# Optimization experiments

Hardware: AMD Instinct MI355X
Metric: run time of the kernel (lower is better)

Reference implementation:

```python
import jax, jax.numpy as jnp
import numpy as np

SHAPE = (128, 128, 128)  # (D, H, W), batch_size = 1
N = 100000               # number of active voxels
CONV_CH = [(3, 64), (64, 64), (64, 96), (96, 96), (96, 128), (128, 128),
           (128, 160), (160, 160), (160, 192), (192, 192), (192, 224),
           (224, 224), (224, 256), (256, 256)]


def _lin(c, shape):
    Sz, Sy, Sx = shape
    return ((c[:, 0] * Sz + c[:, 1]) * Sy + c[:, 2]) * Sx + c[:, 3]


def _subm_pairs(coords, shape):
    # Submanifold conv indice pairs: for each active voxel and each of the
    # 27 kernel offsets, the row index of the active neighbor, or -1.
    Sz, Sy, Sx = shape
    n = coords.shape[0]
    grid = np.full(Sz * Sy * Sx, -1, np.int64)  # batch size 1 dense lookup (like self.grid)
    grid[_lin(coords, shape)] = np.arange(n)
    pairs = []
    for dz in (-1, 0, 1):
        for dy in (-1, 0, 1):
            for dx in (-1, 0, 1):
                z = coords[:, 1] + dz
                y = coords[:, 2] + dy
                x = coords[:, 3] + dx
                ok = (z >= 0) & (z < Sz) & (y >= 0) & (y < Sy) & (x >= 0) & (x < Sx)
                nl = ((coords[:, 0] * Sz + z) * Sy + y) * Sx + x
                pairs.append(np.where(ok, grid[np.clip(nl, 0, grid.size - 1)], -1))
    return np.stack(pairs)  # [27, n]


def _pool_structure(coords, shape):
    # SparseMaxPool3d(2,2): output sites = unique coords//2; inv maps each
    # input voxel to its output window.
    ns = tuple(s // 2 for s in shape)
    c2 = coords.copy()
    c2[:, 1:] = c2[:, 1:] // 2
    key = _lin(c2, ns)
    uniq, inv = np.unique(key, return_inverse=True)
    Sz, Sy, Sx = ns
    b = uniq // (Sz * Sy * Sx)
    r = uniq % (Sz * Sy * Sx)
    z = r // (Sy * Sx)
    r = r % (Sy * Sx)
    nc = np.stack([b, z, r // Sx, r % Sx], 1).astype(np.int64)
    return nc, inv, uniq.shape[0], ns


def _build_plan(coors_np):
    # Paired SubMConv3d layers share an indice_key -> same pairs per level.
    coords = coors_np.astype(np.int64)
    shape = SHAPE
    plan = []
    for lvl in range(7):
        p = jnp.asarray(_subm_pairs(coords, shape))
        plan.append(('conv', p))
        plan.append(('conv', p))
        if lvl < 6:
            coords, inv, m, shape = _pool_structure(coords, shape)
            plan.append(('pool', jnp.asarray(inv), m))
    return plan


def _subm_conv(feats, pairs, W):
    # gather -> GEMM -> accumulate, per kernel offset (W: [27, Cin, Cout])
    out = jnp.zeros((feats.shape[0], W.shape[2]), feats.dtype)
    for k in range(27):
        idx = pairs[k]
        g = jnp.where((idx >= 0)[:, None], feats[jnp.clip(idx, 0)], 0.0)
        out = out + g @ W[k]
    return out


def _forward(feats, weights, plan):
    wi = 0
    for step in plan:
        if step[0] == 'conv':
            feats = _subm_conv(feats, step[1], weights[wi])
            wi += 1
        else:
            feats = jax.ops.segment_max(feats, step[1], num_segments=step[2])
    return feats


def setup_inputs() -> dict:
    rng = np.random.default_rng(0)
    lin = rng.choice(SHAPE[0] * SHAPE[1] * SHAPE[2], size=N, replace=False)
    z = lin // (SHAPE[1] * SHAPE[2])
    r = lin % (SHAPE[1] * SHAPE[2])
    coors = np.stack([np.zeros(N, np.int32), z.astype(np.int32),
                      (r // SHAPE[2]).astype(np.int32), (r % SHAPE[2]).astype(np.int32)], 1)
    key = jax.random.key(0)
    keys = jax.random.split(key, len(CONV_CH) + 1)
    inp = {
        'features': jax.random.normal(keys[0], (N, 3), jnp.float32),
        'coors': jnp.asarray(coors),
        'batch_size': 1,
    }
    for i, (ci, co) in enumerate(CONV_CH):
        inp[f'w{i}'] = jax.random.normal(keys[i + 1], (27, ci, co), jnp.float32) * (1.0 / np.sqrt(27.0 * ci))
    return inp


def reference(features, coors, batch_size, w0, w1, w2, w3, w4, w5, w6, w7, w8, w9, w10, w11, w12, w13):
    plan = _build_plan(np.asarray(coors))
    ws = [w0, w1, w2, w3, w4, w5, w6, w7, w8, w9, w10, w11, w12, w13]
    return _forward(features, ws, plan)
```

## Files before the change

kernel.cpp:

```cpp
#include <hip/hip_runtime.h>
#include <cstdint>
#include <cstddef>


typedef __attribute__((ext_vector_type(8))) short short8v;
typedef __attribute__((ext_vector_type(4))) float f32x4;

static inline int cdiv_h(int a, int b) { return (a + b - 1) / b; }

__device__ inline unsigned short f2bf(float f) {
    unsigned int u = __builtin_bit_cast(unsigned int, f);
    u += 0x7FFFu + ((u >> 16) & 1u);
    return (unsigned short)(u >> 16);
}
__device__ inline float bf2f(unsigned short h) {
    unsigned int u = ((unsigned int)h) << 16;
    return __builtin_bit_cast(float, u);
}

__device__ inline void gload_lds16(const void* g, void* l) {
    auto gp = (const __attribute__((address_space(1))) unsigned int*)(uintptr_t)g;
    auto lp = (__attribute__((address_space(3))) unsigned int*)(uintptr_t)l;
    __builtin_amdgcn_global_load_lds(gp, lp, 16, 0, 0);
}

__device__ inline int xcd_swz(int bid, int nwg) {
    int q = nwg >> 3, r = nwg & 7;
    int x = bid & 7, idx = bid >> 3;
    return (x < r ? x * (q + 1) : r * (q + 1) + (x - r) * q) + idx;
}

__global__ void set_count_k(int* counts, int n) { counts[0] = n; }

__global__ void scatter_grid_k(const int* __restrict__ coords, const int* __restrict__ cnt,
                               int* __restrict__ grid, int S)
{
    int i = blockIdx.x * blockDim.x + threadIdx.x;
    if (i >= cnt[0]) return;
    int z = coords[i * 4 + 1], y = coords[i * 4 + 2], x = coords[i * 4 + 3];
    grid[(z * S + y) * S + x] = i;
}

__global__ void build_pairs_k(const int* __restrict__ coords, const int* __restrict__ cnt,
                              const int* __restrict__ grid, int* __restrict__ pairs_t, int S)
{
    int i = blockIdx.x * blockDim.x + threadIdx.x;
    if (i >= cnt[0]) return;
    int z = coords[i * 4 + 1], y = coords[i * 4 + 2], x = coords[i * 4 + 3];
    int4* dst = reinterpret_cast<int4*>(pairs_t + (size_t)i * 32);
#pragma unroll
    for (int g = 0; g < 7; ++g) {
        int4 q;
#pragma unroll
        for (int j = 0; j < 4; ++j) {
            int k = g * 4 + j;
            int v = -1;
            if (k < 27) {
                int nz = z + k / 9 - 1;
                int ny = y + (k / 3) % 3 - 1;
                int nx = x + k % 3 - 1;
                if (nz >= 0 && nz < S && ny >= 0 && ny < S && nx >= 0 && nx < S)
                    v = grid[(nz * S + ny) * S + nx];
            }
            ((int*)&q)[j] = v;
        }
        dst[g] = q;
    }
}

struct PackArgs {
    const float* src[13];
    unsigned short* dst[13];
    int cin[13];
    int cout[13];
    int tileStart[14];
};

__global__ __launch_bounds__(256) void pack_all_k(PackArgs pa)
{
    int g = blockIdx.x * 4 + ((int)threadIdx.x >> 6);
    int lane = (int)threadIdx.x & 63;
    if (g >= pa.tileStart[13]) return;
    int li = 0;
    while (li < 12 && g >= pa.tileStart[li + 1]) ++li;
    int tile = g - pa.tileStart[li];
    int CIN = pa.cin[li], COUT = pa.cout[li];
    int NS = CIN >> 5, NT = COUT >> 4;
    int t = tile % NT;
    int s = (tile / NT) % NS;
    int k = tile / (NT * NS);
    int kabs = s * 32 + (lane >> 4) * 8;
    int c = t * 16 + (lane & 15);
    const float* src = pa.src[li] + ((size_t)(k * CIN + kabs)) * COUT + c;
    unsigned short* dst = pa.dst[li] + (size_t)tile * 512 + lane * 8;
#pragma unroll
    for (int j = 0; j < 8; ++j) dst[j] = f2bf(src[(size_t)j * COUT]);
}

__global__ __launch_bounds__(256) void conv0_k(
    const float* __restrict__ fin, const float* __restrict__ W,
    const int* __restrict__ pairs_t, const int* __restrict__ cnt,
    unsigned short* __restrict__ fout)
{
    const int row = blockIdx.x * 16 + ((int)threadIdx.x >> 4);
    const int cg = ((int)threadIdx.x & 15) * 4;
    if (row >= cnt[0]) return;
    float a0 = 0, a1 = 0, a2 = 0, a3 = 0;
    for (int k = 0; k < 27; ++k) {
        int nb = pairs_t[(size_t)row * 32 + k];
        if (nb < 0) continue;
        const float* fr = fin + (size_t)nb * 3;
        const float* wk = W + (size_t)k * 3 * 64 + cg;
#pragma unroll
        for (int ci = 0; ci < 3; ++ci) {
            float f = fr[ci];
            float4 w = *reinterpret_cast<const float4*>(wk + ci * 64);
            a0 += f * w.x; a1 += f * w.y; a2 += f * w.z; a3 += f * w.w;
        }
    }
    size_t o = (size_t)row * 64 + cg;
    fout[o] = f2bf(a0); fout[o + 1] = f2bf(a1);
    fout[o + 2] = f2bf(a2); fout[o + 3] = f2bf(a3);
}

template <int CIN, int COUT, int RT, int CT, int GY, bool OUTF32>
__global__ __launch_bounds__(256) void conv_lds_k(
    const unsigned short* __restrict__ fin, const unsigned short* __restrict__ Wp,
    const int* __restrict__ pairs_t, const int* __restrict__ cnt,
    void* __restrict__ fout)
{
    constexpr int NS = CIN / 32, NT = COUT / 16;
    constexpr int NCH = NS * CT;
    __shared__ unsigned short sB[2][NCH * 512];

    const int lane = (int)threadIdx.x & 63;
    const int wave = (int)threadIdx.x >> 6;
    const int l15 = lane & 15, lhi = lane >> 4;
    const int M = cnt[0];

    const int lid = xcd_swz((int)blockIdx.x, (int)gridDim.x);
    const int rowBlock = lid / GY;
    const int ct0 = (lid % GY) * CT;
    const int rowBase = (rowBlock * 4 + wave) * (RT * 16);

    const unsigned short* __restrict__ finL = fin + (size_t)lhi * 8;

    f32x4 acc[RT][CT];
#pragma unroll
    for (int a = 0; a < RT; ++a)
#pragma unroll
        for (int b = 0; b < CT; ++b) acc[a][b] = (f32x4){0.f, 0.f, 0.f, 0.f};

    int  rowC[RT];
    bool rOK[RT];
#pragma unroll
    for (int rt = 0; rt < RT; ++rt) {
        int r = rowBase + rt * 16 + l15;
        rOK[rt]  = r < M;
        rowC[rt] = rOK[rt] ? r : 0;
    }

#define STAGE(K, BUF)                                                              \
    {                                                                              \
        const unsigned short* srcB = Wp + (size_t)(K) * (NS * NT * 512)            \
                                     + (size_t)lane * 8;                           \
        _Pragma("unroll") for (int ii = 0; ii < (NCH + 3) / 4; ++ii) {             \
            int idx = wave + ii * 4;                                               \
            if (idx < NCH) {                                                       \
                int s = idx / CT, tt = idx % CT;                                   \
                gload_lds16(srcB + ((size_t)s * NT + ct0 + tt) * 512,              \
                            &sB[BUF][idx * 512]);                                  \
            }                                                                      \
        }                                                                          \
    }

#define GATHER(AARR, NBARR, KT)                                                    \
    {                                                                              \
        _Pragma("unroll") for (int rt = 0; rt < RT; ++rt)                          \
            NBARR[rt] = rOK[rt] ? pairs_t[(size_t)rowC[rt] * 32 + (KT)] : -1;      \
        _Pragma("unroll") for (int s = 0; s < NS; ++s)                             \
        _Pragma("unroll") for (int rt = 0; rt < RT; ++rt) {                        \
            AARR[s][rt] = (short8v){};                                             \
            if (NBARR[rt] >= 0)                                                    \
                AARR[s][rt] = *reinterpret_cast<const short8v*>(                   \
                    finL + (size_t)NBARR[rt] * CIN + s * 32);                      \
        }                                                                          \
    }

#define COMPUTE(AARR, NBARR, BUF)                                                  \
    {                                                                              \
        int act[RT]; bool anyAct = false;                                          \
        _Pragma("unroll") for (int rt = 0; rt < RT; ++rt) {                        \
            act[rt] = __any(NBARR[rt] >= 0);                                       \
            anyAct = anyAct || (act[rt] != 0);                                     \
        }                                                                          \
        if (anyAct) {                                                              \
            const unsigned short* __restrict__ buf = sB[BUF];                      \
            _Pragma("unroll") for (int s = 0; s < NS; ++s) {                       \
                short8v bb[CT];                                                    \
                _Pragma("unroll") for (int t = 0; t < CT; ++t)                     \
                    bb[t] = *reinterpret_cast<const short8v*>(                     \
                        &buf[(s * CT + t) * 512 + lane * 8]);                      \
                _Pragma("unroll") for (int rt = 0; rt < RT; ++rt) {                \
                    if (!act[rt]) continue;                                        \
                    _Pragma("unroll") for (int t = 0; t < CT; ++t)                 \
                        acc[rt][t] = __builtin_amdgcn_mfma_f32_16x16x32_bf16(      \
                            AARR[s][rt], bb[t], acc[rt][t], 0, 0, 0);              \
                }                                                                  \
            }                                                                      \
        }                                                                          \
    }

    int nbP[RT], nbQ[RT];
    short8v aP[NS][RT], aQ[NS][RT];

    GATHER(aP, nbP, 0);
    STAGE(0, 0);

    for (int kk = 0; kk < 13; ++kk) {
        const int k1 = 2 * kk + 1;
        __syncthreads();
        STAGE(k1, 1);
        GATHER(aQ, nbQ, k1);
        COMPUTE(aP, nbP, 0);
        __syncthreads();
        STAGE(k1 + 1, 0);
        GATHER(aP, nbP, k1 + 1);
        COMPUTE(aQ, nbQ, 1);
    }
    __syncthreads();
    COMPUTE(aP, nbP, 0);

#undef STAGE
#undef GATHER
#undef COMPUTE

#pragma unroll
    for (int rt = 0; rt < RT; ++rt) {
#pragma unroll
        for (int j = 0; j < 4; ++j) {
            int r = rowBase + rt * 16 + lhi * 4 + j;
            if (r >= M) continue;
#pragma unroll
            for (int t = 0; t < CT; ++t) {
                int c = (ct0 + t) * 16 + l15;
                if constexpr (OUTF32)
                    ((float*)fout)[(size_t)r * COUT + c] = acc[rt][t][j];
                else
                    ((unsigned short*)fout)[(size_t)r * COUT + c] = f2bf(acc[rt][t][j]);
            }
        }
    }
}

template <int CIN, int COUT, int CTD, int TG>
__global__ __launch_bounds__(64) void conv_deep_k(
    const unsigned short* __restrict__ fin, const unsigned short* __restrict__ Wp,
    const int* __restrict__ pairs_t, const int* __restrict__ cnt,
    float* __restrict__ fout)
{
    constexpr int NS = CIN / 32, NT = COUT / 16;
    const int lane = (int)threadIdx.x;
    const int l15 = lane & 15, lhi = lane >> 4;
    const int M = cnt[0];
    if ((int)blockIdx.x * 16 >= M) return;
    const int row = blockIdx.x * 16 + l15;
    const int ct0 = blockIdx.y * CTD;
    const int k0 = blockIdx.z * TG;

    f32x4 acc[CTD];
#pragma unroll
    for (int t = 0; t < CTD; ++t) acc[t] = (f32x4){0.f, 0.f, 0.f, 0.f};

    bool anyTap = false;
#pragma unroll
    for (int kk = 0; kk < TG; ++kk) {
        const int k = k0 + kk;
        int nb = (row < M) ? pairs_t[(size_t)row * 32 + k] : -1;
        if (!__any(nb >= 0)) continue;
        anyTap = true;
        const unsigned short* wk = Wp + (size_t)k * NS * NT * 512 + (size_t)lane * 8;

        short8v a[NS];
#pragma unroll
        for (int s = 0; s < NS; ++s) {
            a[s] = (short8v){};
            if (nb >= 0)
                a[s] = *reinterpret_cast<const short8v*>(
                    fin + (size_t)nb * CIN + s * 32 + lhi * 8);
        }
#pragma unroll
        for (int s = 0; s < NS; ++s)
#pragma unroll
            for (int t = 0; t < CTD; ++t) {
                short8v b = *reinterpret_cast<const short8v*>(
                    wk + ((size_t)s * NT + ct0 + t) * 512);
                acc[t] = __builtin_amdgcn_mfma_f32_16x16x32_bf16(a[s], b, acc[t], 0, 0, 0);
            }
    }
    if (!anyTap) return;

#pragma unroll
    for (int t = 0; t < CTD; ++t)
#pragma unroll
        for (int j = 0; j < 4; ++j) {
            int r = blockIdx.x * 16 + lhi * 4 + j;
            if (r < M)
                atomicAdd(&fout[(size_t)r * COUT + (ct0 + t) * 16 + l15], acc[t][j]);
        }
}

__global__ __launch_bounds__(256) void f32_to_bf16_k(
    const float* __restrict__ src, const int* __restrict__ cnt,
    unsigned short* __restrict__ dst, int C)
{
    int idx = blockIdx.x * 256 + (int)threadIdx.x;
    if (idx / C >= cnt[0]) return;
    dst[idx] = f2bf(src[idx]);
}

__global__ void mark_occ_k(const int* __restrict__ coords, const int* __restrict__ cnt,
                           int* __restrict__ occ, int Sh)
{
    int i = blockIdx.x * blockDim.x + threadIdx.x;
    if (i >= cnt[0]) return;
    int z = coords[i * 4 + 1] >> 1, y = coords[i * 4 + 2] >> 1, x = coords[i * 4 + 3] >> 1;
    occ[(z * Sh + y) * Sh + x] = 1;
}

__global__ __launch_bounds__(256) void scan_sum_k(const int* __restrict__ occ, int P,
                                                  int* __restrict__ bsum)
{
    int base = blockIdx.x * 4096 + (int)threadIdx.x * 16;
    int s = 0;
#pragma unroll
    for (int j = 0; j < 16; ++j) { int i = base + j; s += (i < P) ? occ[i] : 0; }
    for (int off = 1; off < 64; off <<= 1) s += __shfl_xor(s, off);
    __shared__ int ws[4];
    if ((threadIdx.x & 63) == 0) ws[threadIdx.x >> 6] = s;
    __syncthreads();
    if (threadIdx.x == 0) bsum[blockIdx.x] = ws[0] + ws[1] + ws[2] + ws[3];
}

__global__ void scan_offsets_k(const int* __restrict__ bsum, int nb,
                               int* __restrict__ boff, int* __restrict__ cntOut)
{
    int lane = threadIdx.x;
    int v = (lane < nb) ? bsum[lane] : 0;
    int incl = v;
    for (int off = 1; off < 64; off <<= 1) {
        int t = __shfl_up(incl, off);
        if (lane >= off) incl += t;
    }
    if (lane < nb) boff[lane] = incl - v;
    if (lane == 63) cntOut[0] = incl;
}

__global__ __launch_bounds__(256) void scan_emit_k(const int* __restrict__ occ, int P,
                                                   const int* __restrict__ boff,
                                                   int* __restrict__ newcoords, int Sh)
{
    __shared__ int ws[4];
    int tid = threadIdx.x;
    int base = blockIdx.x * 4096 + tid * 16;
    int v[16];
    int s = 0;
#pragma unroll
    for (int j = 0; j < 16; ++j) { int i = base + j; v[j] = (i < P) ? occ[i] : 0; s += v[j]; }
    int mysum = s;
    int incl = s;
    for (int off = 1; off < 64; off <<= 1) {
        int t = __shfl_up(incl, off);
        if ((tid & 63) >= off) incl += t;
    }
    if ((tid & 63) == 63) ws[tid >> 6] = incl;
    __syncthreads();
    int waveOff = 0;
    for (int w = 0; w < (tid >> 6); ++w) waveOff += ws[w];
    int r = boff[blockIdx.x] + waveOff + incl - mysum;
    const int SS = Sh * Sh;
#pragma unroll
    for (int j = 0; j < 16; ++j) {
        if (v[j]) {
            int c = base + j;
            newcoords[r * 4 + 0] = 0;
            newcoords[r * 4 + 1] = c / SS;
            newcoords[r * 4 + 2] = (c % SS) / Sh;
            newcoords[r * 4 + 3] = c % Sh;
            ++r;
        }
    }
}

__global__ void pool_max_k(const unsigned short* __restrict__ fin, const int* __restrict__ gridPrev,
                           const int* __restrict__ newcoords, const int* __restrict__ cnt,
                           unsigned short* __restrict__ fout, int C, int Sprev)
{
    int idx = blockIdx.x * blockDim.x + threadIdx.x;
    int r = idx / C, c = idx % C;
    if (r >= cnt[0]) return;
    int z2 = newcoords[r * 4 + 1] * 2;
    int y2 = newcoords[r * 4 + 2] * 2;
    int x2 = newcoords[r * 4 + 3] * 2;
    float best = -3.4e38f;
    unsigned short bb = 0;
#pragma unroll
    for (int d = 0; d < 8; ++d) {
        int z = z2 + (d >> 2), y = y2 + ((d >> 1) & 1), x = x2 + (d & 1);
        int j = gridPrev[(z * Sprev + y) * Sprev + x];
        if (j >= 0) {
            unsigned short u = fin[(size_t)j * C + c];
            float f = bf2f(u);
            if (f > best) { best = f; bb = u; }
        }
    }
    fout[(size_t)r * C + c] = bb;
}


template <int CIN, int COUT, int RT, int CT, int GY, bool OUTF32>
static void launch_cl(const unsigned short* fin, const unsigned short* Wp,
                      const int* pairs_t, const int* cnt, void* fout,
                      int bound, hipStream_t stream)
{
    constexpr int NT = COUT / 16;
    static_assert(CIN % 32 == 0 && COUT % 16 == 0 && CT * GY == NT, "shape");
    dim3 g(cdiv_h(bound, RT * 64) * GY);
    conv_lds_k<CIN, COUT, RT, CT, GY, OUTF32><<<g, 256, 0, stream>>>(fin, Wp, pairs_t,
                                                                     cnt, fout);
}

template <int CIN, int COUT, int CTD, int TG>
static void launch_deep(const unsigned short* fin, const unsigned short* Wp,
                        const int* pairs_t, const int* cnt, float* acc,
                        int bound, hipStream_t stream)
{
    constexpr int NT = COUT / 16;
    static_assert(NT % CTD == 0 && 27 % TG == 0, "shape");
    dim3 g(cdiv_h(bound, 16), NT / CTD, 27 / TG);
    conv_deep_k<CIN, COUT, CTD, TG><<<g, 64, 0, stream>>>(fin, Wp, pairs_t, cnt, acc);
}

extern "C" void kernel_launch(void* const* d_in, const int* in_sizes, int n_in,
                              void* d_out, int out_size, void* d_ws, size_t ws_size,
                              hipStream_t stream)
{
    const float* feats0 = (const float*)d_in[0];
    const int*   coors  = (const int*)d_in[1];
    const float* w[14];
    for (int i = 0; i < 14; ++i) w[i] = (const float*)d_in[3 + i];
    float* out = (float*)d_out;
    const int N = in_sizes[0] / 3;

    char* p = (char*)d_ws;
    int* grid   = (int*)p; p += (size_t)128 * 128 * 128 * 4;
    int* occ    = (int*)p; p += (size_t)64 * 64 * 64 * 4;
    int* counts = (int*)p; p += 256;
    int* bsum   = (int*)p; p += 256;
    int* boff   = (int*)p; p += 256;
    int* pairs_t = (int*)p; p += (size_t)N * 32 * 4;
    int* coordsA = (int*)p; p += (size_t)N * 16;
    int* coordsB = (int*)p; p += (size_t)N * 16;
    unsigned short* featA = (unsigned short*)p; p += (size_t)N * 96 * 2;
    unsigned short* featB = (unsigned short*)p; p += (size_t)N * 96 * 2;
    float* scratch = (float*)p; p += (size_t)4096 * 192 * 4;
    unsigned short* wpBase = (unsigned short*)p;

    static const int CH[14][2] = {{3,64},{64,64},{64,96},{96,96},{96,128},{128,128},
                                  {128,160},{160,160},{160,192},{192,192},{192,224},
                                  {224,224},{224,256},{256,256}};
    unsigned short* wp[14];
    PackArgs pa;
    {
        size_t off = 0;
        int ts = 0;
        for (int i = 1; i < 14; ++i) {
            wp[i] = wpBase + off;
            off += (size_t)27 * CH[i][0] * CH[i][1];
            pa.src[i - 1] = w[i];
            pa.dst[i - 1] = wp[i];
            pa.cin[i - 1] = CH[i][0];
            pa.cout[i - 1] = CH[i][1];
            pa.tileStart[i - 1] = ts;
            ts += 27 * (CH[i][0] / 32) * (CH[i][1] / 16);
        }
        pa.tileStart[13] = ts;
    }

    int bounds[7];
    for (int l = 0; l < 7; ++l) {
        int S = 128 >> l, c = S * S * S;
        bounds[l] = N < c ? N : c;
    }

    set_count_k<<<1, 1, 0, stream>>>(counts, N);
    hipMemsetAsync(d_out, 0, (size_t)out_size * 4, stream);
    pack_all_k<<<cdiv_h(pa.tileStart[13], 4), 256, 0, stream>>>(pa);

    auto build_level = [&](const int* coordsL, int lvl) {
        int S = 128 >> lvl;
        hipMemsetAsync(grid, 0xFF, (size_t)S * S * S * 4, stream);
        int blocks = cdiv_h(bounds[lvl], 256);
        scatter_grid_k<<<blocks, 256, 0, stream>>>(coordsL, counts + lvl, grid, S);
        build_pairs_k<<<blocks, 256, 0, stream>>>(coordsL, counts + lvl, grid, pairs_t, S);
    };

    auto do_pool = [&](const int* coordsL, int lvl, const unsigned short* fin,
                       unsigned short* fout, int C, int* coordsOut) {
        int S = 128 >> lvl, Sh = S / 2, P = Sh * Sh * Sh;
        hipMemsetAsync(occ, 0, (size_t)P * 4, stream);
        mark_occ_k<<<cdiv_h(bounds[lvl], 256), 256, 0, stream>>>(coordsL, counts + lvl, occ, Sh);
        int nb = cdiv_h(P, 4096);
        scan_sum_k<<<nb, 256, 0, stream>>>(occ, P, bsum);
        scan_offsets_k<<<1, 64, 0, stream>>>(bsum, nb, boff, counts + lvl + 1);
        scan_emit_k<<<nb, 256, 0, stream>>>(occ, P, boff, coordsOut, Sh);
        int total = bounds[lvl + 1] * C;
        pool_max_k<<<cdiv_h(total, 256), 256, 0, stream>>>(fin, grid, coordsOut,
                                                           counts + lvl + 1, fout, C, S);
    };

    auto deep_conv = [&](auto launcher, const unsigned short* fin, int wi, int lvl,
                         unsigned short* dst, int COUT) {
        hipMemsetAsync(scratch, 0, (size_t)bounds[lvl] * COUT * 4, stream);
        launcher(fin, wp[wi], pairs_t, counts + lvl, scratch, bounds[lvl], stream);
        f32_to_bf16_k<<<cdiv_h(bounds[lvl] * COUT, 256), 256, 0, stream>>>(
            scratch, counts + lvl, dst, COUT);
    };

    build_level(coors, 0);
    conv0_k<<<cdiv_h(bounds[0], 16), 256, 0, stream>>>(feats0, w[0], pairs_t, counts + 0, featA);
    launch_cl<64, 64, 2, 4, 1, false>(featA, wp[1], pairs_t, counts + 0, featB, bounds[0], stream);
    do_pool(coors, 0, featB, featA, 64, coordsA);
    build_level(coordsA, 1);
    launch_cl<64, 96, 2, 6, 1, false>(featA, wp[2], pairs_t, counts + 1, featB, bounds[1], stream);
    launch_cl<96, 96, 2, 6, 1, false>(featB, wp[3], pairs_t, counts + 1, featA, bounds[1], stream);
    do_pool(coordsA, 1, featA, featB, 96, coordsB);
    build_level(coordsB, 2);
    launch_cl<96, 128, 2, 4, 2, false>(featB, wp[4], pairs_t, counts + 2, featA, bounds[2], stream);
    launch_cl<128, 128, 2, 4, 2, false>(featA, wp[5], pairs_t, counts + 2, featB, bounds[2], stream);
    do_pool(coordsB, 2, featB, featA, 128, coordsA);
    build_level(coordsA, 3);
    deep_conv(launch_deep<128, 160, 2, 3>, featA, 6, 3, featB, 160);
    deep_conv(launch_deep<160, 160, 2, 3>, featB, 7, 3, featA, 160);
    do_pool(coordsA, 3, featA, featB, 160, coordsB);
    build_level(coordsB, 4);
    deep_conv(launch_deep<160, 192, 2, 3>, featB, 8, 4, featA, 192);
    deep_conv(launch_deep<192, 192, 2, 3>, featA, 9, 4, featB, 192);
    do_pool(coordsB, 4, featB, featA, 192, coordsA);
    build_level(coordsA, 5);
    deep_conv(launch_deep<192, 224, 1, 1>, featA, 10, 5, featB, 224);
    deep_conv(launch_deep<224, 224, 1, 1>, featB, 11, 5, featA, 224);
    do_pool(coordsA, 5, featA, featB, 224, coordsB);
    build_level(coordsB, 6);
    deep_conv(launch_deep<224, 256, 1, 1>, featB, 12, 6, featA, 256);
    launch_deep<256, 256, 1, 1>(featA, wp[13], pairs_t, counts + 6, out, bounds[6], stream);
}
```

Before: 774.7 us.

## Triple-buffer weight LDS staging with counted vmcnt waits and unconditional gathers

Moves the sparse conv kernel from a double-buffered, __syncthreads-separated loop to a three-slot LDS ring for weight tiles. Weight loads and neighbour gathers for the next offset stay in flight across the barrier, using an explicit s_waitcnt vmcnt with a fixed outstanding count. Every stage and gather now issues a uniform number of loads: invalid neighbours read row 0 and are masked, and out-of-range stages write to a dummy LDS buffer, so the count holds. Blocks whose rows are all past M now exit early. In exchange the kernel uses more LDS and registers, which may lower occupancy, and it does extra wasted loads.

```diff
diff --git a/kernel.cpp b/kernel.cpp
--- a/kernel.cpp
+++ b/kernel.cpp
@@ -131,7 +131,12 @@
 {
     constexpr int NS = CIN / 32, NT = COUT / 16;
     constexpr int NCH = NS * CT;
-    __shared__ unsigned short sB[2][NCH * 512];
+    constexpr int SPW = (NCH + 3) / 4;
+    constexpr int G   = NS * RT;
+    constexpr int XW  = SPW + 2 * G + 2 * RT;
+    static_assert(XW <= 63, "vmcnt range");
+    __shared__ unsigned short sB[3][NCH * 512];
+    __shared__ unsigned short sDummy[512];
 
     const int lane = (int)threadIdx.x & 63;
     const int wave = (int)threadIdx.x >> 6;
@@ -141,6 +146,7 @@
     const int lid = xcd_swz((int)blockIdx.x, (int)gridDim.x);
     const int rowBlock = lid / GY;
     const int ct0 = (lid % GY) * CT;
+    if (rowBlock * (RT * 64) >= M) return;
     const int rowBase = (rowBlock * 4 + wave) * (RT * 16);
 
     const unsigned short* __restrict__ finL = fin + (size_t)lhi * 8;
@@ -160,79 +166,114 @@
         rowC[rt] = rOK[rt] ? r : 0;
     }
 
-#define STAGE(K, BUF)                                                              \
+#define STAGE(K, BUFP)                                                             \
     {                                                                              \
-        const unsigned short* srcB = Wp + (size_t)(K) * (NS * NT * 512)            \
+        const int kc_ = (K) > 26 ? 26 : (K);                                       \
+        const bool real_ = (K) <= 26;                                              \
+        const unsigned short* srcB = Wp + (size_t)kc_ * (NS * NT * 512)            \
                                      + (size_t)lane * 8;                           \
-        _Pragma("unroll") for (int ii = 0; ii < (NCH + 3) / 4; ++ii) {             \
+        _Pragma("unroll") for (int ii = 0; ii < SPW; ++ii) {                       \
             int idx = wave + ii * 4;                                               \
-            if (idx < NCH) {                                                       \
-                int s = idx / CT, tt = idx % CT;                                   \
-                gload_lds16(srcB + ((size_t)s * NT + ct0 + tt) * 512,              \
-                            &sB[BUF][idx * 512]);                                  \
-            }                                                                      \
+            int cidx = idx < NCH ? idx : 0;                                        \
+            int s_ = cidx / CT, tt_ = cidx % CT;                                   \
+            unsigned short* dst = (real_ && idx < NCH)                             \
+                                      ? ((BUFP) + idx * 512) : sDummy;             \
+            gload_lds16(srcB + ((size_t)s_ * NT + ct0 + tt_) * 512, dst);          \
         }                                                                          \
     }
 
-#define GATHER(AARR, NBARR, KT)                                                    \
+#define NBLOAD(NB, K)                                                              \
     {                                                                              \
+        _Pragma("unroll") for (int rt = 0; rt < RT; ++rt) {                        \
+            int t_ = pairs_t[(size_t)rowC[rt] * 32 + (K)];                         \
+            NB[rt] = rOK[rt] ? t_ : -1;                                            \
+        }                                                                          \
+    }
+
+#define GATHER(AARR, NB)                                                           \
+    {                                                                              \
+        _Pragma("unroll") for (int s_ = 0; s_ < NS; ++s_)                          \
+        _Pragma("unroll") for (int rt = 0; rt < RT; ++rt) {                        \
+            int n_ = NB[rt] < 0 ? 0 : NB[rt];                                      \
+            short8v v_ = *reinterpret_cast<const short8v*>(                        \
+                finL + (size_t)n_ * CIN + s_ * 32);                                \
+            AARR[s_][rt] = NB[rt] < 0 ? (short8v){} : v_;                          \
+        }                                                                          \
+    }
+
+#define WAITBAR                                                                    \
+    asm volatile("s_waitcnt vmcnt(%0)" :: "n"(XW) : "memory");                     \
+    __builtin_amdgcn_s_barrier();                                                  \
+    asm volatile("" ::: "memory");
+
+#define COMPUTE(AARR, ACT, BUFP)                                                   \
+    {                                                                              \
+        bool anyAct = false;                                                       \
         _Pragma("unroll") for (int rt = 0; rt < RT; ++rt)                          \
-            NBARR[rt] = rOK[rt] ? pairs_t[(size_t)rowC[rt] * 32 + (KT)] : -1;      \
-        _Pragma("unroll") for (int s = 0; s < NS; ++s)                             \
-        _Pragma("unroll") for (int rt = 0; rt < RT; ++rt) {                        \
-            AARR[s][rt] = (short8v){};                                             \
-            if (NBARR[rt] >= 0)                                                    \
-                AARR[s][rt] = *reinterpret_cast<const short8v*>(                   \
-                    finL + (size_t)NBARR[rt] * CIN + s * 32);                      \
-        }                                                                          \
-    }
-
-#define COMPUTE(AARR, NBARR, BUF)                                                  \
-    {                                                                              \
-        int act[RT]; bool anyAct = false;                                          \
-        _Pragma("unroll") for (int rt = 0; rt < RT; ++rt) {                        \
-            act[rt] = __any(NBARR[rt] >= 0);                                       \
-            anyAct = anyAct || (act[rt] != 0);                                     \
-        }                                                                          \
+            anyAct = anyAct || (ACT[rt] != 0);                                     \
         if (anyAct) {                                                              \
-            const unsigned short* __restrict__ buf = sB[BUF];                      \
-            _Pragma("unroll") for (int s = 0; s < NS; ++s) {                       \
+            const unsigned short* __restrict__ buf = (BUFP);                       \
+            _Pragma("unroll") for (int s_ = 0; s_ < NS; ++s_) {                    \
                 short8v bb[CT];                                                    \
-                _Pragma("unroll") for (int t = 0; t < CT; ++t)                     \
-                    bb[t] = *reinterpret_cast<const short8v*>(                     \
-                        &buf[(s * CT + t) * 512 + lane * 8]);                      \
+                _Pragma("unroll") for (int t_ = 0; t_ < CT; ++t_)                  \
+                    bb[t_] = *reinterpret_cast<const short8v*>(                    \
+                        &buf[(s_ * CT + t_) * 512 + lane * 8]);                    \
                 _Pragma("unroll") for (int rt = 0; rt < RT; ++rt) {                \
-                    if (!act[rt]) continue;                                        \
-                    _Pragma("unroll") for (int t = 0; t < CT; ++t)                 \
-                        acc[rt][t] = __builtin_amdgcn_mfma_f32_16x16x32_bf16(      \
-                            AARR[s][rt], bb[t], acc[rt][t], 0, 0, 0);              \
+                    if (!ACT[rt]) continue;                                        \
+                    _Pragma("unroll") for (int t_ = 0; t_ < CT; ++t_)              \
+                        acc[rt][t_] = __builtin_amdgcn_mfma_f32_16x16x32_bf16(     \
+                            AARR[s_][rt], bb[t_], acc[rt][t_], 0, 0, 0);           \
                 }                                                                  \
             }                                                                      \
         }                                                                          \
     }
 
-    int nbP[RT], nbQ[RT];
-    short8v aP[NS][RT], aQ[NS][RT];
-
-    GATHER(aP, nbP, 0);
-    STAGE(0, 0);
-
+    int nbE[RT], nbO[RT];
+    short8v aE[NS][RT], aO[NS][RT];
+
+    NBLOAD(nbE, 0);
+    STAGE(0, &sB[0][0]);
+    GATHER(aE, nbE);
+    NBLOAD(nbO, 1);
+
+    int bcur = 0;
     for (int kk = 0; kk < 13; ++kk) {
-        const int k1 = 2 * kk + 1;
-        __syncthreads();
-        STAGE(k1, 1);
-        GATHER(aQ, nbQ, k1);
-        COMPUTE(aP, nbP, 0);
-        __syncthreads();
-        STAGE(k1 + 1, 0);
-        GATHER(aP, nbP, k1 + 1);
-        COMPUTE(aQ, nbQ, 1);
-    }
-    __syncthreads();
-    COMPUTE(aP, nbP, 0);
+        const int k0 = 2 * kk;
+        const int bn1 = bcur + 1 > 2 ? bcur - 2 : bcur + 1;
+        const int bn2 = bn1 + 1 > 2 ? bn1 - 2 : bn1 + 1;
+        STAGE(k0 + 1, &sB[bn1][0]);
+        GATHER(aO, nbO);
+        int actE[RT];
+#pragma unroll
+        for (int rt = 0; rt < RT; ++rt) actE[rt] = __any(nbE[rt] >= 0);
+        NBLOAD(nbE, k0 + 2);
+        WAITBAR;
+        COMPUTE(aE, actE, &sB[bcur][0]);
+        STAGE(k0 + 2, &sB[bn2][0]);
+        GATHER(aE, nbE);
+        int actO[RT];
+#pragma unroll
+        for (int rt = 0; rt < RT; ++rt) actO[rt] = __any(nbO[rt] >= 0);
+        NBLOAD(nbO, k0 + 3);
+        WAITBAR;
+        COMPUTE(aO, actO, &sB[bn1][0]);
+        bcur = bn2;
+    }
+    {
+        STAGE(27, &sB[0][0]);
+        GATHER(aO, nbO);
+        int actT[RT];
+#pragma unroll
+        for (int rt = 0; rt < RT; ++rt) actT[rt] = __any(nbE[rt] >= 0);
+        NBLOAD(nbO, 28);
+        WAITBAR;
+        COMPUTE(aE, actT, &sB[bcur][0]);
+    }
 
 #undef STAGE
+#undef NBLOAD
 #undef GATHER
+#undef WAITBAR
 #undef COMPUTE
 
 #pragma unroll
```

Result: no change. 763.8 us (-1.4%).
